# Kernel optimization log

Measured on AMD Instinct MI355X. Metric: run time of the kernel, lower is better.

Reference implementation:

```python
import jax, jax.numpy as jnp
import numpy as np

N_NODES = 100000
N_EDGES = 300000
N_TYPES = 3
HID = 128
EMB = 64
N_GRAPHS = 4096
T_STEPS = 4


def setup_inputs() -> dict:
    key = jax.random.key(0)
    ks = jax.random.split(key, 12)
    s = 1.0 / np.sqrt(HID)
    return {
        "node_features": jax.random.normal(ks[0], (N_NODES, HID), jnp.float32),
        "edge_index": jax.random.randint(ks[1], (N_TYPES, 2, N_EDGES), 0, N_NODES),
        "node_to_graph_id": jnp.sort(jax.random.randint(ks[2], (N_NODES,), 0, N_GRAPHS)),
        "W_msg": jax.random.normal(ks[3], (N_TYPES, HID, HID), jnp.float32) * s,
        "b_msg": jnp.zeros((N_TYPES, HID), jnp.float32),
        "W_ih": jax.random.normal(ks[4], (3 * HID, HID), jnp.float32) * s,
        "W_hh": jax.random.normal(ks[5], (3 * HID, HID), jnp.float32) * s,
        "b_ih": jnp.zeros((3 * HID,), jnp.float32),
        "b_hh": jnp.zeros((3 * HID,), jnp.float32),
        "W_proj": jax.random.normal(ks[6], (EMB, HID), jnp.float32) * s,
        "b_proj": jnp.zeros((EMB,), jnp.float32),
        "W_gate": jax.random.normal(ks[7], (EMB, HID), jnp.float32) * s,
        "b_gate": jnp.zeros((EMB,), jnp.float32),
    }


def _gru_cell(m, h, W_ih, W_hh, b_ih, b_hh):
    # torch.nn.GRUCell math; gates ordered (r, z, n)
    gi = m @ W_ih.T + b_ih          # [N, 3H]
    gh = h @ W_hh.T + b_hh          # [N, 3H]
    i_r, i_z, i_n = jnp.split(gi, 3, axis=-1)
    h_r, h_z, h_n = jnp.split(gh, 3, axis=-1)
    r = jax.nn.sigmoid(i_r + h_r)
    z = jax.nn.sigmoid(i_z + h_z)
    n = jnp.tanh(i_n + r * h_n)
    return (1.0 - z) * n + z * h


def reference(node_features, edge_index, node_to_graph_id,
              W_msg, b_msg, W_ih, W_hh, b_ih, b_hh,
              W_proj, b_proj, W_gate, b_gate):
    h = node_features  # [N, H]

    def per_type(eidx, W, b, h):
        src, dst = eidx[0], eidx[1]
        m = h[src] @ W + b  # gather + per-edge-type linear, [E, H]
        return jax.ops.segment_sum(m, dst, num_segments=N_NODES)

    for _ in range(T_STEPS):  # fixed small T: python loop is fine
        msgs = jax.vmap(per_type, in_axes=(0, 0, 0, None))(edge_index, W_msg, b_msg, h)
        m = msgs.sum(axis=0)  # [N, H] aggregated over edge types
        h = _gru_cell(m, h, W_ih, W_hh, b_ih, b_hh)

    # gated index_add graph readout (mlp_down is identity)
    proj = h @ W_proj.T + b_proj                 # [N, E]
    gate = jax.nn.sigmoid(h @ W_gate.T + b_gate)  # [N, E]
    graph_feats = jax.ops.segment_sum(gate * proj, node_to_graph_id,
                                      num_segments=N_GRAPHS)
    return graph_feats
```

## Files before the change

### kernel.cpp

```cpp
#include <hip/hip_runtime.h>
#include <hip/hip_bf16.h>
#include <math.h>

#define NN 100000
#define NNP 100096
#define NE 300000
#define HID 128
#define EMB 64
#define NG 4096
#define DEG_CAP 32
#define XS 512

typedef __bf16 bf16x8 __attribute__((ext_vector_type(8)));
typedef float  f32x16 __attribute__((ext_vector_type(16)));
typedef short  short8 __attribute__((ext_vector_type(8)));

__device__ __forceinline__ float bf2f(unsigned short u) {
    unsigned int x = ((unsigned int)u) << 16;
    return __builtin_bit_cast(float, x);
}
__device__ __forceinline__ unsigned short f2bf(float f) {
    unsigned int x = __builtin_bit_cast(unsigned int, f);
    unsigned int r = x + 0x7fff + ((x >> 16) & 1);
    return (unsigned short)(r >> 16);
}
__device__ __forceinline__ float sigm(float x) { return 1.f / (1.f + __expf(-x)); }

__global__ __launch_bounds__(256) void k_init(const float* __restrict__ nf,
                                              unsigned short* __restrict__ X) {
    int id = blockIdx.x * 256 + threadIdx.x;
    int n = id >> 7, c = id & 127;
    X[(long)n * XS + 384 + c] = f2bf(nf[id]);
}

__global__ __launch_bounds__(256) void k_build_csr(const int* __restrict__ ei,
                                                   int* __restrict__ deg,
                                                   int* __restrict__ csr) {
    int id = blockIdx.x * 256 + threadIdx.x;
    if (id >= 3 * NE) return;
    int t = id / NE;
    int i = id - t * NE;
    int src = ei[(t * 2 + 0) * NE + i];
    int dst = ei[(t * 2 + 1) * NE + i];
    int p = atomicAdd(&deg[t * NN + dst], 1);
    if (p < DEG_CAP) csr[((long)t * NN + dst) * DEG_CAP + p] = src;
}

__global__ __launch_bounds__(256) void k_pack_deg(const int* __restrict__ deg,
                                                  int4* __restrict__ degp) {
    int n = blockIdx.x * 256 + threadIdx.x;
    if (n >= NNP) return;
    int4 v; v.x = 0; v.y = 0; v.z = 0; v.w = 0;
    if (n < NN) { v.x = deg[n]; v.y = deg[NN + n]; v.z = deg[2 * NN + n]; }
    degp[n] = v;
}

__global__ __launch_bounds__(512) void k_build_w(const float* __restrict__ Wmsg,
                                                 const float* __restrict__ Wih,
                                                 const float* __restrict__ Whh,
                                                 unsigned short* __restrict__ Wnk) {
    int n = blockIdx.x;
    int k = threadIdx.x;
    int sec = n >> 7, c = n & 127;
    float v = 0.f;
    if (k < 384) {
        if (sec < 3) {
            int t = k >> 7, kk = k & 127;
            const float* wm = Wmsg + ((long)t * HID + kk) * HID;
            const float* wi = Wih + (long)(sec * HID + c) * HID;
            float s = 0.f;
            for (int j = 0; j < HID; j++) s += wm[j] * wi[j];
            v = s;
        }
    } else {
        int kk = k - 384;
        if (sec == 0)      v = Whh[(long)c * HID + kk];
        else if (sec == 1) v = Whh[(long)(HID + c) * HID + kk];
        else if (sec == 3) v = Whh[(long)(2 * HID + c) * HID + kk];
    }
    Wnk[(long)n * 512 + k] = f2bf(v);
}

__global__ __launch_bounds__(512) void k_build_bias(const float* __restrict__ bih,
                                                    const float* __restrict__ bhh,
                                                    const float* __restrict__ bmsg,
                                                    const float* __restrict__ Wih,
                                                    float* __restrict__ bbig,
                                                    float* __restrict__ Bdeg) {
    int n = threadIdx.x;
    int sec = n >> 7, c = n & 127;
    float b;
    if (sec == 0)      b = bih[c] + bhh[c];
    else if (sec == 1) b = bih[HID + c] + bhh[HID + c];
    else if (sec == 2) b = bih[2 * HID + c];
    else               b = bhh[2 * HID + c];
    bbig[n] = b;
    for (int t = 0; t < 3; t++) {
        float s = 0.f;
        if (sec < 3) {
            const float* wi = Wih + (long)(sec * HID + c) * HID;
            const float* bm = bmsg + t * HID;
            for (int j = 0; j < HID; j++) s += bm[j] * wi[j];
        }
        Bdeg[t * 512 + n] = s;
    }
}

__global__ __launch_bounds__(256) void k_agg(unsigned short* __restrict__ X,
                                             const int* __restrict__ deg,
                                             const int* __restrict__ csr) {
    const int lane = threadIdx.x & 63;
    const long n = (long)blockIdx.x * 4 + (threadIdx.x >> 6);
    const int g = lane >> 4;
    const int c16 = lane & 15;
    const int l31 = lane & 31;

    int d[3], il[3];
#pragma unroll
    for (int t = 0; t < 3; t++) {
        int dt = deg[t * NN + n];
        d[t] = dt > DEG_CAP ? DEG_CAP : dt;
        il[t] = csr[((long)t * NN + n) * DEG_CAP + l31];
    }
#pragma unroll
    for (int t = 0; t < 3; t++) {
        float acc[8] = {0.f, 0.f, 0.f, 0.f, 0.f, 0.f, 0.f, 0.f};
        int rounds = (d[t] + 3) >> 2;
        for (int r = 0; r < rounds; r++) {
            int j = r * 4 + g;
            int idx = __shfl(il[t], j & 31);
            if (j < d[t]) {
                short8 v = *(const short8*)(X + (long)idx * XS + 384 + c16 * 8);
#pragma unroll
                for (int q = 0; q < 8; q++) acc[q] += bf2f((unsigned short)v[q]);
            }
        }
#pragma unroll
        for (int q = 0; q < 8; q++) {
            acc[q] += __shfl_xor(acc[q], 16);
            acc[q] += __shfl_xor(acc[q], 32);
        }
        if (g == 0) {
            short8 o;
#pragma unroll
            for (int q = 0; q < 8; q++) o[q] = (short)f2bf(acc[q]);
            *(short8*)(X + n * XS + t * HID + c16 * 8) = o;
        }
    }
}

__global__ __launch_bounds__(512, 2) void k_gru_mfma(
        unsigned short* __restrict__ X, const unsigned short* __restrict__ Wnk,
        const float* __restrict__ bbig, const float* __restrict__ Bdeg,
        const int4* __restrict__ degp) {
    __shared__ char lds[40960];
    char* Al = lds;
    char* Bl = lds + 8192;

    const int tid = threadIdx.x;
    const int lane = tid & 63;
    const int wv = tid >> 6;
    const int wr = wv >> 2;
    const int wc = wv & 3;
    const int r31 = lane & 31;
    const int kg = lane >> 5;
    const int swr = (r31 >> 1) & 3;
    const long row0 = (long)blockIdx.x * 128;

    f32x16 acc[2][4];
#pragma unroll
    for (int i = 0; i < 2; i++)
#pragma unroll
        for (int j = 0; j < 4; j++) acc[i][j] = (f32x16)(0.0f);

    const int srow = tid >> 2;
    const int su = tid & 3;
    const int swu = (su ^ ((srow >> 1) & 3)) * 16;
    const char* pA = (const char*)X + (row0 + srow) * 1024 + swu;
    const char* pB = (const char*)Wnk + (long)srow * 1024 + swu;

    float4 pa, pb0, pb1, pb2, pb3;
    pa  = *(const float4*)(pA);
    pb0 = *(const float4*)(pB);
    pb1 = *(const float4*)(pB + 131072);
    pb2 = *(const float4*)(pB + 262144);
    pb3 = *(const float4*)(pB + 393216);

    for (int it = 0; it < 16; it++) {
        __syncthreads();
        *(float4*)(Al + tid * 16)         = pa;
        *(float4*)(Bl + tid * 16)         = pb0;
        *(float4*)(Bl + 8192  + tid * 16) = pb1;
        *(float4*)(Bl + 16384 + tid * 16) = pb2;
        *(float4*)(Bl + 24576 + tid * 16) = pb3;
        if (it < 15) {
            long ko = (long)(it + 1) * 64;
            pa  = *(const float4*)(pA + ko);
            pb0 = *(const float4*)(pB + ko);
            pb1 = *(const float4*)(pB + 131072 + ko);
            pb2 = *(const float4*)(pB + 262144 + ko);
            pb3 = *(const float4*)(pB + 393216 + ko);
        }
        __syncthreads();

        short8 af[2][2], bfr[4][2];
#pragma unroll
        for (int rt = 0; rt < 2; rt++)
#pragma unroll
            for (int kb = 0; kb < 2; kb++)
                af[rt][kb] = *(const short8*)(Al + (wr * 64 + rt * 32 + r31) * 64 +
                                              (((2 * kb + kg) ^ swr) * 16));
#pragma unroll
        for (int ct = 0; ct < 4; ct++)
#pragma unroll
            for (int kb = 0; kb < 2; kb++)
                bfr[ct][kb] = *(const short8*)(Bl + (wc * 128 + ct * 32 + r31) * 64 +
                                               (((2 * kb + kg) ^ swr) * 16));
#pragma unroll
        for (int kb = 0; kb < 2; kb++)
#pragma unroll
            for (int rt = 0; rt < 2; rt++)
#pragma unroll
                for (int ct = 0; ct < 4; ct++)
                    acc[rt][ct] = __builtin_amdgcn_mfma_f32_32x32x16_bf16(
                        __builtin_bit_cast(bf16x8, af[rt][kb]),
                        __builtin_bit_cast(bf16x8, bfr[ct][kb]),
                        acc[rt][ct], 0, 0, 0);
    }

    float* EX = (float*)lds;
#pragma unroll
    for (int ch = 0; ch < 8; ch++) {
        __syncthreads();
        if (wr == (ch >> 2)) {
            const int rt = (ch >> 1) & 1;
            const int half = ch & 1;
#pragma unroll
            for (int ct = 0; ct < 4; ct++) {
                int n = wc * 128 + ct * 32 + r31;
#pragma unroll
                for (int q = 0; q < 8; q++) {
                    int row16 = (q & 3) + 8 * ((q >> 2) & 1) + 4 * kg;
                    EX[row16 * 512 + n] = acc[rt][ct][half * 8 + q];
                }
            }
        }
        __syncthreads();
        {
            int row16 = tid >> 5;
            int c0 = (tid & 31) << 2;
            long grow = row0 + ch * 16 + row16;
            int4 dg = degp[grow];
            float dgx = (float)dg.x, dgy = (float)dg.y, dgz = (float)dg.z;
            const float* ex = EX + row16 * 512;
            float4 vr = *(const float4*)(ex + c0);
            float4 vz = *(const float4*)(ex + 128 + c0);
            float4 vn = *(const float4*)(ex + 256 + c0);
            float4 vh = *(const float4*)(ex + 384 + c0);
            float4 br = *(const float4*)(bbig + c0);
            float4 bz = *(const float4*)(bbig + 128 + c0);
            float4 bn = *(const float4*)(bbig + 256 + c0);
            float4 bh = *(const float4*)(bbig + 384 + c0);
            float4 d00 = *(const float4*)(Bdeg + c0);
            float4 d01 = *(const float4*)(Bdeg + 128 + c0);
            float4 d02 = *(const float4*)(Bdeg + 256 + c0);
            float4 d10 = *(const float4*)(Bdeg + 512 + c0);
            float4 d11 = *(const float4*)(Bdeg + 512 + 128 + c0);
            float4 d12 = *(const float4*)(Bdeg + 512 + 256 + c0);
            float4 d20 = *(const float4*)(Bdeg + 1024 + c0);
            float4 d21 = *(const float4*)(Bdeg + 1024 + 128 + c0);
            float4 d22 = *(const float4*)(Bdeg + 1024 + 256 + c0);
            ushort4 ho = *(const ushort4*)(X + grow * XS + 384 + c0);

            float aR[4] = {vr.x, vr.y, vr.z, vr.w};
            float aZ[4] = {vz.x, vz.y, vz.z, vz.w};
            float aN[4] = {vn.x, vn.y, vn.z, vn.w};
            float aH[4] = {vh.x, vh.y, vh.z, vh.w};
            float bR[4] = {br.x, br.y, br.z, br.w};
            float bZ[4] = {bz.x, bz.y, bz.z, bz.w};
            float bN[4] = {bn.x, bn.y, bn.z, bn.w};
            float bH[4] = {bh.x, bh.y, bh.z, bh.w};
            float e00[4] = {d00.x, d00.y, d00.z, d00.w};
            float e01[4] = {d01.x, d01.y, d01.z, d01.w};
            float e02[4] = {d02.x, d02.y, d02.z, d02.w};
            float e10[4] = {d10.x, d10.y, d10.z, d10.w};
            float e11[4] = {d11.x, d11.y, d11.z, d11.w};
            float e12[4] = {d12.x, d12.y, d12.z, d12.w};
            float e20[4] = {d20.x, d20.y, d20.z, d20.w};
            float e21[4] = {d21.x, d21.y, d21.z, d21.w};
            float e22[4] = {d22.x, d22.y, d22.z, d22.w};
            unsigned short hold[4] = {ho.x, ho.y, ho.z, ho.w};

            ushort4 outp;
            unsigned short* op = (unsigned short*)&outp;
#pragma unroll
            for (int cc = 0; cc < 4; cc++) {
                float Sr = aR[cc] + bR[cc] + dgx * e00[cc] + dgy * e10[cc] + dgz * e20[cc];
                float Sz = aZ[cc] + bZ[cc] + dgx * e01[cc] + dgy * e11[cc] + dgz * e21[cc];
                float In = aN[cc] + bN[cc] + dgx * e02[cc] + dgy * e12[cc] + dgz * e22[cc];
                float Hn = aH[cc] + bH[cc];
                float rr = sigm(Sr);
                float zz = sigm(Sz);
                float tt = In + rr * Hn;
                float e2 = __expf(2.f * tt);
                float nn = 1.f - 2.f / (e2 + 1.f);
                float hv = (1.f - zz) * nn + zz * bf2f(hold[cc]);
                op[cc] = f2bf(hv);
            }
            *(ushort4*)(X + grow * XS + 384 + c0) = outp;
        }
    }
}

__global__ __launch_bounds__(256) void k_readout(const unsigned short* __restrict__ X,
                                                 const int* __restrict__ n2g,
                                                 const float* __restrict__ Wp,
                                                 const float* __restrict__ bp,
                                                 const float* __restrict__ Wg,
                                                 const float* __restrict__ bg,
                                                 float* __restrict__ out) {
    __shared__ float hs[32][132];
    __shared__ float Ws[64][129];
    int tid = threadIdx.x;
    long row0 = (long)blockIdx.x * 32;
    int rg = tid >> 5, cg = tid & 31;
    float acc[4][4];
#pragma unroll
    for (int r = 0; r < 4; r++)
#pragma unroll
        for (int c = 0; c < 4; c++) acc[r][c] = 0.f;

#pragma unroll
    for (int p = 0; p < 2; p++) {
        int e = p * 256 + tid;
        int r = e >> 4, c8 = e & 15;
        short8 v = *(const short8*)(X + (row0 + r) * XS + 384 + c8 * 8);
#pragma unroll
        for (int j = 0; j < 8; j++) hs[r][c8 * 8 + j] = bf2f((unsigned short)v[j]);
    }
    for (int kc = 0; kc < 128; kc += 64) {
        __syncthreads();
#pragma unroll
        for (int p = 0; p < 8; p++) {
            int idx = p * 256 + tid;
            int j = idx >> 4, q = idx & 15;
            const float* Wsrc = (j < 64) ? Wp : Wg;
            float4 w = *(const float4*)&Wsrc[(j & 63) * HID + kc + q * 4];
            Ws[q * 4 + 0][j] = w.x;
            Ws[q * 4 + 1][j] = w.y;
            Ws[q * 4 + 2][j] = w.z;
            Ws[q * 4 + 3][j] = w.w;
        }
        __syncthreads();
#pragma unroll 8
        for (int k = 0; k < 64; k++) {
            float a[4], w[4];
#pragma unroll
            for (int r = 0; r < 4; r++) a[r] = hs[rg * 4 + r][kc + k];
#pragma unroll
            for (int c = 0; c < 4; c++) w[c] = Ws[k][cg + 32 * c];
#pragma unroll
            for (int r = 0; r < 4; r++)
#pragma unroll
                for (int c = 0; c < 4; c++) acc[r][c] += a[r] * w[c];
        }
    }
#pragma unroll
    for (int r = 0; r < 4; r++) {
        long row = row0 + rg * 4 + r;
        if (row < NN) {
            int g = n2g[row];
            float pv0 = acc[r][0] + bp[cg];
            float pv1 = acc[r][1] + bp[cg + 32];
            float gv0 = acc[r][2] + bg[cg];
            float gv1 = acc[r][3] + bg[cg + 32];
            atomicAdd(&out[g * EMB + cg],      pv0 * sigm(gv0));
            atomicAdd(&out[g * EMB + cg + 32], pv1 * sigm(gv1));
        }
    }
}

extern "C" void kernel_launch(void* const* d_in, const int* in_sizes, int n_in,
                              void* d_out, int out_size, void* d_ws, size_t ws_size,
                              hipStream_t stream) {
    const float* node_features = (const float*)d_in[0];
    const int*   edge_index    = (const int*)d_in[1];
    const int*   n2g           = (const int*)d_in[2];
    const float* W_msg         = (const float*)d_in[3];
    const float* b_msg         = (const float*)d_in[4];
    const float* W_ih          = (const float*)d_in[5];
    const float* W_hh          = (const float*)d_in[6];
    const float* b_ih          = (const float*)d_in[7];
    const float* b_hh          = (const float*)d_in[8];
    const float* W_proj        = (const float*)d_in[9];
    const float* b_proj        = (const float*)d_in[10];
    const float* W_gate        = (const float*)d_in[11];
    const float* b_gate        = (const float*)d_in[12];

    char* ws = (char*)d_ws;
    unsigned short* X    = (unsigned short*)(ws);
    unsigned short* Wnk  = (unsigned short*)(ws + 102498304);
    float*          bbig = (float*)         (ws + 103022592);
    float*          Bdeg = (float*)         (ws + 103024640);
    int4*           degp = (int4*)          (ws + 103030784);
    int*            deg  = (int*)           (ws + 104632320);
    int*            csr  = (int*)           (ws + 105832320);

    float* out = (float*)d_out;

    hipMemsetAsync(out, 0, (size_t)NG * EMB * sizeof(float), stream);
    hipMemsetAsync(deg, 0, (size_t)3 * NN * sizeof(int), stream);

    k_init<<<dim3((NN * HID) / 256), dim3(256), 0, stream>>>(node_features, X);
    k_build_csr<<<dim3((3 * NE + 255) / 256), dim3(256), 0, stream>>>(edge_index, deg, csr);
    k_pack_deg<<<dim3(NNP / 256), dim3(256), 0, stream>>>(deg, degp);
    k_build_w<<<dim3(512), dim3(512), 0, stream>>>(W_msg, W_ih, W_hh, Wnk);
    k_build_bias<<<dim3(1), dim3(512), 0, stream>>>(b_ih, b_hh, b_msg, W_ih, bbig, Bdeg);

    for (int step = 0; step < 4; step++) {
        k_agg<<<dim3(NN / 4), dim3(256), 0, stream>>>(X, deg, csr);
        k_gru_mfma<<<dim3(NNP / 128), dim3(512), 0, stream>>>(X, Wnk, bbig, Bdeg, degp);
    }
    k_readout<<<dim3(NN / 32), dim3(256), 0, stream>>>(X, n2g, W_proj, b_proj,
                                                       W_gate, b_gate, out);
}
```

Before: 940.6 us.

## Double-buffer GRU GEMM tiles with direct global-to-LDS loads

The GRU MFMA kernel's K-loop now fetches the next A and B tiles with global_load_lds straight into a second LDS buffer, instead of staging them through registers and writing them to LDS. This removes the register round trip and one of the two barriers per iteration, so the loads overlap with the MFMA work on the current buffer. In exchange, LDS per block doubles to 80 KB, which could limit occupancy. Correctness now depends on the barrier also waiting for the asynchronous LDS loads to finish. The X pointer is also split into a const read alias and a separate write alias, although both receive the same buffer.

```diff
diff --git a/kernel.cpp b/kernel.cpp
--- a/kernel.cpp
+++ b/kernel.cpp
@@ -14,6 +14,13 @@
 typedef __bf16 bf16x8 __attribute__((ext_vector_type(8)));
 typedef float  f32x16 __attribute__((ext_vector_type(16)));
 typedef short  short8 __attribute__((ext_vector_type(8)));
+
+typedef const __attribute__((address_space(1))) unsigned int* gas_u32;
+typedef __attribute__((address_space(3))) unsigned int* las_u32;
+
+__device__ __forceinline__ void gload16(const void* g, void* l) {
+    __builtin_amdgcn_global_load_lds((gas_u32)g, (las_u32)l, 16, 0, 0);
+}
 
 __device__ __forceinline__ float bf2f(unsigned short u) {
     unsigned int x = ((unsigned int)u) << 16;
@@ -150,12 +157,11 @@
 }
 
 __global__ __launch_bounds__(512, 2) void k_gru_mfma(
-        unsigned short* __restrict__ X, const unsigned short* __restrict__ Wnk,
+        const unsigned short* __restrict__ X, unsigned short* __restrict__ Xw,
+        const unsigned short* __restrict__ Wnk,
         const float* __restrict__ bbig, const float* __restrict__ Bdeg,
         const int4* __restrict__ degp) {
-    __shared__ char lds[40960];
-    char* Al = lds;
-    char* Bl = lds + 8192;
+    __shared__ char lds[81920];
 
     const int tid = threadIdx.x;
     const int lane = tid & 63;
@@ -178,30 +184,33 @@
     const int swu = (su ^ ((srow >> 1) & 3)) * 16;
     const char* pA = (const char*)X + (row0 + srow) * 1024 + swu;
     const char* pB = (const char*)Wnk + (long)srow * 1024 + swu;
-
-    float4 pa, pb0, pb1, pb2, pb3;
-    pa  = *(const float4*)(pA);
-    pb0 = *(const float4*)(pB);
-    pb1 = *(const float4*)(pB + 131072);
-    pb2 = *(const float4*)(pB + 262144);
-    pb3 = *(const float4*)(pB + 393216);
-
+    const int wvb = wv * 1024;
+
+    {
+        char* Ad = &lds[wvb];
+        char* Bd = &lds[8192 + wvb];
+        gload16(pA, Ad);
+        gload16(pB, Bd);
+        gload16(pB + 131072, Bd + 8192);
+        gload16(pB + 262144, Bd + 16384);
+        gload16(pB + 393216, Bd + 24576);
+    }
+
+    int cur = 0;
     for (int it = 0; it < 16; it++) {
         __syncthreads();
-        *(float4*)(Al + tid * 16)         = pa;
-        *(float4*)(Bl + tid * 16)         = pb0;
-        *(float4*)(Bl + 8192  + tid * 16) = pb1;
-        *(float4*)(Bl + 16384 + tid * 16) = pb2;
-        *(float4*)(Bl + 24576 + tid * 16) = pb3;
         if (it < 15) {
             long ko = (long)(it + 1) * 64;
-            pa  = *(const float4*)(pA + ko);
-            pb0 = *(const float4*)(pB + ko);
-            pb1 = *(const float4*)(pB + 131072 + ko);
-            pb2 = *(const float4*)(pB + 262144 + ko);
-            pb3 = *(const float4*)(pB + 393216 + ko);
-        }
-        __syncthreads();
+            char* Ad = &lds[(cur ^ 1) * 40960 + wvb];
+            char* Bd = &lds[(cur ^ 1) * 40960 + 8192 + wvb];
+            gload16(pA + ko, Ad);
+            gload16(pB + ko, Bd);
+            gload16(pB + 131072 + ko, Bd + 8192);
+            gload16(pB + 262144 + ko, Bd + 16384);
+            gload16(pB + 393216 + ko, Bd + 24576);
+        }
+        const char* Al = &lds[cur * 40960];
+        const char* Bl = &lds[cur * 40960 + 8192];
 
         short8 af[2][2], bfr[4][2];
 #pragma unroll
@@ -226,6 +235,7 @@
                         __builtin_bit_cast(bf16x8, af[rt][kb]),
                         __builtin_bit_cast(bf16x8, bfr[ct][kb]),
                         acc[rt][ct], 0, 0, 0);
+        cur ^= 1;
     }
 
     float* EX = (float*)lds;
@@ -307,7 +317,7 @@
                 float hv = (1.f - zz) * nn + zz * bf2f(hold[cc]);
                 op[cc] = f2bf(hv);
             }
-            *(ushort4*)(X + grow * XS + 384 + c0) = outp;
+            *(ushort4*)(Xw + grow * XS + 384 + c0) = outp;
         }
     }
 }
@@ -419,7 +429,7 @@
 
     for (int step = 0; step < 4; step++) {
         k_agg<<<dim3(NN / 4), dim3(256), 0, stream>>>(X, deg, csr);
-        k_gru_mfma<<<dim3(NNP / 128), dim3(512), 0, stream>>>(X, Wnk, bbig, Bdeg, degp);
+        k_gru_mfma<<<dim3(NNP / 128), dim3(512), 0, stream>>>(X, X, Wnk, bbig, Bdeg, degp);
     }
     k_readout<<<dim3(NN / 32), dim3(256), 0, stream>>>(X, n2g, W_proj, b_proj,
                                                        W_gate, b_gate, out);
```

Result: no change. 952.2 us (+1.2%).
